# Kernel tuning notes

Hardware: AMD Instinct MI355X
Metric: run time of the kernel (lower is better)

The kernel has to match this reference:

```python
import jax, jax.numpy as jnp
import numpy as np

B, T, WARM, H, FIN, MLPW = 8192, 30, 24, 128, 8, 128
WX = ['clouds','pres','precip','temp','rh','ghi','wind_x','wind_y']
TL = ['hour_sin','hour_cos','year_sin','year_cos','elev_angle','azimuth_sin','azimuth_cos']


def setup_inputs() -> dict:
    key = jax.random.key(0)
    ks = jax.random.split(key, 32)
    d = {}
    for i, n in enumerate(WX + TL):
        d[n] = jax.random.normal(ks[i], (B, T), dtype=jnp.float32)
    d['irradiance_in'] = jax.random.uniform(ks[20], (B, WARM), dtype=jnp.float32)
    s = lambda fan: 1.0 / np.sqrt(fan).astype(np.float32)
    # LSTM params (flax OptimizedLSTMCell math: fused input/hidden kernels, one bias), gate order i,f,g,o
    d['Wi'] = jax.random.normal(ks[21], (FIN, 4 * H), dtype=jnp.float32) * s(FIN)
    d['Wh'] = jax.random.normal(ks[22], (H, 4 * H), dtype=jnp.float32) * s(H)
    d['b'] = jnp.zeros((4 * H,), jnp.float32)
    # output head: MLP(depth=2, width=128) with relu, then Dense(1)
    d['W1'] = jax.random.normal(ks[23], (H, MLPW), dtype=jnp.float32) * s(H)
    d['b1'] = jnp.zeros((MLPW,), jnp.float32)
    d['W2'] = jax.random.normal(ks[24], (MLPW, MLPW), dtype=jnp.float32) * s(MLPW)
    d['b2'] = jnp.zeros((MLPW,), jnp.float32)
    d['Wout'] = jax.random.normal(ks[25], (MLPW, 1), dtype=jnp.float32) * s(MLPW)
    d['bout'] = jnp.zeros((1,), jnp.float32)
    return d


def reference(clouds, pres, precip, temp, rh, ghi, wind_x, wind_y,
              hour_sin, hour_cos, year_sin, year_cos, elev_angle, azimuth_sin, azimuth_cos,
              irradiance_in, Wi, Wh, b, W1, b1, W2, b2, Wout, bout):
    # FLAGS.weather=False path: x is the time/location feature stack [B, T, 7].
    # Weather features are accepted (as in the original dict) but unused.
    x = jnp.stack([hour_sin, hour_cos, year_sin, year_cos, elev_angle, azimuth_sin, azimuth_cos], axis=-1)
    warm_in = jnp.concatenate([x[:, :WARM], irradiance_in[..., None]], axis=-1)  # [B, 24, 8]
    auto_in = x[:, WARM:]                                                        # [B, 6, 7]

    def lstm_step(c, h, inp):
        z = inp @ Wi + h @ Wh + b                    # [B, 4H]
        i, f, g, o = jnp.split(z, 4, axis=-1)
        c2 = jax.nn.sigmoid(f) * c + jax.nn.sigmoid(i) * jnp.tanh(g)
        h2 = jax.nn.sigmoid(o) * jnp.tanh(c2)
        return c2, h2

    def out_mlp(h):
        h = jax.nn.relu(h @ W1 + b1)
        h = jax.nn.relu(h @ W2 + b2)
        return h @ Wout + bout                       # [..., 1]

    c0 = jnp.zeros((x.shape[0], H), x.dtype)
    h0 = jnp.zeros((x.shape[0], H), x.dtype)

    # warmup: teacher-forced LSTM over observed irradiance
    def warm_step(carry, xt):
        c, h = carry
        c, h = lstm_step(c, h, xt)
        return (c, h), h
    (c, h), hs = jax.lax.scan(warm_step, (c0, h0), jnp.swapaxes(warm_in, 0, 1))
    preds_warm = out_mlp(jnp.swapaxes(hs, 0, 1))     # [B, 24, 1]
    last_pred = preds_warm[:, -1]                    # [B, 1]

    def auto_step(carry, xt):
        c, h, p = carry
        c, h = lstm_step(c, h, jnp.concatenate([xt, p], axis=-1))
        p = out_mlp(h)
        return (c, h, p), p
    _, preds_auto = jax.lax.scan(auto_step, (c, h, last_pred), jnp.swapaxes(auto_in, 0, 1))
    preds_auto = jnp.swapaxes(preds_auto, 0, 1)      # [B, 6, 1]

    pred = jnp.concatenate([preds_warm, preds_auto], axis=1)  # [B, 30, 1]
    return jnp.squeeze(pred, axis=2)                 # [B, 30]
```

## Files before the change

### kernel.cpp

```cpp
#include <hip/hip_runtime.h>


#define T_STEPS 30
#define WARM_N  24

typedef _Float16 h8 __attribute__((ext_vector_type(8)));
typedef __attribute__((ext_vector_type(4))) float float4v;

struct FeatPtrs { const float* f[7]; };

#if __has_builtin(__builtin_amdgcn_rcpf)
#define RCP(x) __builtin_amdgcn_rcpf(x)
#else
#define RCP(x) (1.0f/(x))
#endif

__device__ __forceinline__ float sigm(float x){ return RCP(1.0f + __expf(-x)); }
__device__ __forceinline__ float tanh_(float x){ return 1.0f - 2.0f*RCP(1.0f + __expf(2.0f*x)); }

__global__ void pack_weights(const float* __restrict__ Wi, const float* __restrict__ Wh,
                             const float* __restrict__ W1, const float* __restrict__ W2,
                             _Float16* __restrict__ ws)
{
  int idx = blockIdx.x * 256 + threadIdx.x;
  if (idx >= 224 * 512) return;
  int f    = idx >> 9;
  int r    = idx & 511;
  int lane = r >> 3, j = r & 7;
  int kk   = ((lane >> 4) << 3) + j;
  int c16  = lane & 15;
  float v = 0.0f;
  if (f < 160){
    int wt = f / 20, rem = f % 20, g = rem / 5, ks = rem % 5;
    int col = g * 128 + wt * 16 + c16;
    if (ks == 0) v = (kk < 8) ? Wi[kk * 512 + col] : 0.0f;
    else         v = Wh[((ks - 1) * 32 + kk) * 512 + col];
  } else {
    int f2 = f - 160;
    const float* W = (f2 < 32) ? W1 : W2;
    int f3 = f2 & 31;
    int wt = f3 >> 2, ks = f3 & 3;
    v = W[(ks * 32 + kk) * 128 + wt * 16 + c16];
  }
  ws[idx] = (_Float16)v;
}

__device__ __forceinline__ void head_do(int t, int r0, int step,
    const float* o2s, const float* WoutS, float bout0,
    float* __restrict__ out, float* pS)
{
  if (t < 256){
    int r = t >> 3, jj = t & 7;
    const float* orow = &o2s[r * 132 + jj * 16];
    const float* wrow = &WoutS[jj * 16];
    float s = 0.0f;
#pragma unroll
    for (int q = 0; q < 16; ++q) s += orow[q] * wrow[q];
    s += __shfl_down(s, 4, 8);
    s += __shfl_down(s, 2, 8);
    s += __shfl_down(s, 1, 8);
    if (jj == 0){
      float pv = s + bout0;
      out[(r0 + r) * T_STEPS + step] = pv;
      pS[r] = pv;
    }
  }
}

#define MFMA16 __builtin_amdgcn_mfma_f32_16x16x32_f16

__global__ __launch_bounds__(512, 2)
void lstm_mfma(FeatPtrs fp, const float* __restrict__ irr,
               const _Float16* __restrict__ wsb,
               const float* __restrict__ bz, const float* __restrict__ b1,
               const float* __restrict__ b2, const float* __restrict__ Wout,
               const float* __restrict__ bout, float* __restrict__ out)
{
  __shared__ __align__(16) _Float16 xp[2][1280];
  __shared__ __align__(16) _Float16 hp [4 * 1280];
  __shared__ __align__(16) _Float16 o1p[4 * 1280];
  __shared__ __align__(16) float o2s[32 * 132];
  __shared__ float WoutS[128];
  __shared__ float pS[32];

  const int t   = threadIdx.x;
  const int l   = t & 63;
  const int w   = t >> 6;
  const int c16 = l & 15;
  const int kq  = l >> 4;
  const int r0  = blockIdx.x * 32;

  h8 Bz[4][5], B1f[4], B2f[4];
  {
    const h8* f8 = (const h8*)wsb;
#pragma unroll
    for (int g = 0; g < 4; ++g)
#pragma unroll
      for (int ks = 0; ks < 5; ++ks)
        Bz[g][ks] = f8[((w * 4 + g) * 5 + ks) * 64 + l];
#pragma unroll
    for (int ks = 0; ks < 4; ++ks) B1f[ks] = f8[(160 + w * 4 + ks) * 64 + l];
#pragma unroll
    for (int ks = 0; ks < 4; ++ks) B2f[ks] = f8[(192 + w * 4 + ks) * 64 + l];
  }
  float bzv[4], wi7[4];
#pragma unroll
  for (int g = 0; g < 4; ++g){
    bzv[g] = bz[g * 128 + w * 16 + c16];
    wi7[g] = (float)wsb[((w * 4 + g) * 5) * 512 + c16 * 8 + 7];
  }
  const float b1v   = b1[w * 16 + c16];
  const float b2v   = b2[w * 16 + c16];
  const float bout0 = bout[0];
  if (t < 128) WoutS[t] = Wout[t];

  const float* fbase = nullptr;
  const float* ibase = nullptr;
  int xslot = 0;
  if (t < 256){
    int r = t >> 3, j = t & 7;
    if (j < 7) fbase = fp.f[j] + (r0 + r) * T_STEPS;
    else       ibase = irr + (r0 + r) * WARM_N;
    xslot = (r >> 4) * 640 + (r & 15) * 40 + j;
  }

  {
    int* p = (int*)xp;
    for (int i = t; i < 1280; i += 512) p[i] = 0;
    p = (int*)hp;
    for (int i = t; i < 2560; i += 512) p[i] = 0;
  }

  float cst[8];
#pragma unroll
  for (int i = 0; i < 8; ++i) cst[i] = 0.0f;

  const int aoff = c16 * 40 + kq * 8;
  const int wb   = (w >> 1) * 1280 + (w & 1) * 16 + c16;
  __syncthreads();

  if (t < 256){
    float v0 = fbase ? fbase[0] : ibase[0];
    float v1 = fbase ? fbase[1] : ibase[1];
    xp[0][xslot] = (_Float16)v0;
    xp[1][xslot] = (_Float16)v1;
  }
  __syncthreads();

  for (int i = 0; i < 23; ++i){
    float vnext = 0.0f;
    if (t < 256){
      int step = i + 2;
      if (fbase)               vnext = fbase[step];
      else if (step < WARM_N)  vnext = ibase[step];
    }
    float4v acc[4][2];
#pragma unroll
    for (int g = 0; g < 4; ++g)
#pragma unroll
      for (int m = 0; m < 2; ++m)
#pragma unroll
        for (int r = 0; r < 4; ++r) acc[g][m][r] = bzv[g];
    float4v m1[2];
#pragma unroll
    for (int m = 0; m < 2; ++m)
#pragma unroll
      for (int r = 0; r < 4; ++r) m1[m][r] = b1v;
    {
      const _Float16* xb = xp[i & 1];
      h8 a0 = *(const h8*)&xb[aoff];
      h8 a1 = *(const h8*)&xb[640 + aoff];
#pragma unroll
      for (int g = 0; g < 4; ++g){
        acc[g][0] = MFMA16(a0, Bz[g][0], acc[g][0], 0, 0, 0);
        acc[g][1] = MFMA16(a1, Bz[g][0], acc[g][1], 0, 0, 0);
      }
    }
#pragma unroll
    for (int ks = 0; ks < 4; ++ks){
      h8 ah0 = *(const h8*)&hp[ks * 1280 + aoff];
      h8 ah1 = *(const h8*)&hp[ks * 1280 + 640 + aoff];
#pragma unroll
      for (int g = 0; g < 4; ++g){
        acc[g][0] = MFMA16(ah0, Bz[g][1 + ks], acc[g][0], 0, 0, 0);
        acc[g][1] = MFMA16(ah1, Bz[g][1 + ks], acc[g][1], 0, 0, 0);
      }
      if (i >= 1){
        m1[0] = MFMA16(ah0, B1f[ks], m1[0], 0, 0, 0);
        m1[1] = MFMA16(ah1, B1f[ks], m1[1], 0, 0, 0);
      }
    }
    if (i >= 1){
#pragma unroll
      for (int m = 0; m < 2; ++m)
#pragma unroll
        for (int r = 0; r < 4; ++r)
          o1p[wb + m * 640 + (kq * 4 + r) * 40] = (_Float16)fmaxf(m1[m][r], 0.0f);
    }
    if (i >= 2) head_do(t, r0, i - 2, o2s, WoutS, bout0, out, pS);
    __syncthreads();

    if (t < 256) xp[i & 1][xslot] = (_Float16)vnext;
#pragma unroll
    for (int m = 0; m < 2; ++m)
#pragma unroll
      for (int r = 0; r < 4; ++r){
        float zi = acc[0][m][r], zf = acc[1][m][r], zg = acc[2][m][r], zo = acc[3][m][r];
        float c2 = sigm(zf) * cst[m * 4 + r] + sigm(zi) * tanh_(zg);
        cst[m * 4 + r] = c2;
        float h2 = sigm(zo) * tanh_(c2);
        hp[wb + m * 640 + (kq * 4 + r) * 40] = (_Float16)h2;
      }
    if (i >= 1){
      float4v m2[2];
#pragma unroll
      for (int m = 0; m < 2; ++m)
#pragma unroll
        for (int r = 0; r < 4; ++r) m2[m][r] = b2v;
#pragma unroll
      for (int ks = 0; ks < 4; ++ks){
        h8 a0 = *(const h8*)&o1p[ks * 1280 + aoff];
        h8 a1 = *(const h8*)&o1p[ks * 1280 + 640 + aoff];
        m2[0] = MFMA16(a0, B2f[ks], m2[0], 0, 0, 0);
        m2[1] = MFMA16(a1, B2f[ks], m2[1], 0, 0, 0);
      }
#pragma unroll
      for (int m = 0; m < 2; ++m)
#pragma unroll
        for (int r = 0; r < 4; ++r)
          o2s[(m * 16 + kq * 4 + r) * 132 + w * 16 + c16] = fmaxf(m2[m][r], 0.0f);
    }
    __syncthreads();
  }

  head_do(t, r0, 21, o2s, WoutS, bout0, out, pS);
  __syncthreads();

  for (int s = 23; s < T_STEPS; ++s){
    float vnext = 0.0f;
    if (s <= 27 && t < 256 && fbase) vnext = fbase[s + 2];
    float4v acc[4][2];
#pragma unroll
    for (int g = 0; g < 4; ++g)
#pragma unroll
      for (int m = 0; m < 2; ++m)
#pragma unroll
        for (int r = 0; r < 4; ++r) acc[g][m][r] = bzv[g];
    float4v m1[2];
#pragma unroll
    for (int m = 0; m < 2; ++m)
#pragma unroll
      for (int r = 0; r < 4; ++r) m1[m][r] = b1v;
    {
      const _Float16* xb = xp[s & 1];
      h8 a0 = *(const h8*)&xb[aoff];
      h8 a1 = *(const h8*)&xb[640 + aoff];
#pragma unroll
      for (int g = 0; g < 4; ++g){
        acc[g][0] = MFMA16(a0, Bz[g][0], acc[g][0], 0, 0, 0);
        acc[g][1] = MFMA16(a1, Bz[g][0], acc[g][1], 0, 0, 0);
      }
    }
#pragma unroll
    for (int ks = 0; ks < 4; ++ks){
      h8 ah0 = *(const h8*)&hp[ks * 1280 + aoff];
      h8 ah1 = *(const h8*)&hp[ks * 1280 + 640 + aoff];
#pragma unroll
      for (int g = 0; g < 4; ++g){
        acc[g][0] = MFMA16(ah0, Bz[g][1 + ks], acc[g][0], 0, 0, 0);
        acc[g][1] = MFMA16(ah1, Bz[g][1 + ks], acc[g][1], 0, 0, 0);
      }
      m1[0] = MFMA16(ah0, B1f[ks], m1[0], 0, 0, 0);
      m1[1] = MFMA16(ah1, B1f[ks], m1[1], 0, 0, 0);
    }
#pragma unroll
    for (int m = 0; m < 2; ++m)
#pragma unroll
      for (int r = 0; r < 4; ++r)
        o1p[wb + m * 640 + (kq * 4 + r) * 40] = (_Float16)fmaxf(m1[m][r], 0.0f);
    __syncthreads();

    {
      float4v m2[2];
#pragma unroll
      for (int m = 0; m < 2; ++m)
#pragma unroll
        for (int r = 0; r < 4; ++r) m2[m][r] = b2v;
#pragma unroll
      for (int ks = 0; ks < 4; ++ks){
        h8 a0 = *(const h8*)&o1p[ks * 1280 + aoff];
        h8 a1 = *(const h8*)&o1p[ks * 1280 + 640 + aoff];
        m2[0] = MFMA16(a0, B2f[ks], m2[0], 0, 0, 0);
        m2[1] = MFMA16(a1, B2f[ks], m2[1], 0, 0, 0);
      }
#pragma unroll
      for (int m = 0; m < 2; ++m)
#pragma unroll
        for (int r = 0; r < 4; ++r)
          o2s[(m * 16 + kq * 4 + r) * 132 + w * 16 + c16] = fmaxf(m2[m][r], 0.0f);
    }
    __syncthreads();

    head_do(t, r0, s - 1, o2s, WoutS, bout0, out, pS);
    __syncthreads();

    if (s <= 27 && t < 256) xp[s & 1][xslot] = (_Float16)vnext;
    if (s >= 24){
#pragma unroll
      for (int m = 0; m < 2; ++m)
#pragma unroll
        for (int r = 0; r < 4; ++r){
          float pv = pS[m * 16 + kq * 4 + r];
#pragma unroll
          for (int g = 0; g < 4; ++g) acc[g][m][r] += pv * wi7[g];
        }
    }
#pragma unroll
    for (int m = 0; m < 2; ++m)
#pragma unroll
      for (int r = 0; r < 4; ++r){
        float zi = acc[0][m][r], zf = acc[1][m][r], zg = acc[2][m][r], zo = acc[3][m][r];
        float c2 = sigm(zf) * cst[m * 4 + r] + sigm(zi) * tanh_(zg);
        cst[m * 4 + r] = c2;
        float h2 = sigm(zo) * tanh_(c2);
        hp[wb + m * 640 + (kq * 4 + r) * 40] = (_Float16)h2;
      }
    __syncthreads();
  }

  {
    float4v m1[2];
#pragma unroll
    for (int m = 0; m < 2; ++m)
#pragma unroll
      for (int r = 0; r < 4; ++r) m1[m][r] = b1v;
#pragma unroll
    for (int ks = 0; ks < 4; ++ks){
      h8 ah0 = *(const h8*)&hp[ks * 1280 + aoff];
      h8 ah1 = *(const h8*)&hp[ks * 1280 + 640 + aoff];
      m1[0] = MFMA16(ah0, B1f[ks], m1[0], 0, 0, 0);
      m1[1] = MFMA16(ah1, B1f[ks], m1[1], 0, 0, 0);
    }
#pragma unroll
    for (int m = 0; m < 2; ++m)
#pragma unroll
      for (int r = 0; r < 4; ++r)
        o1p[wb + m * 640 + (kq * 4 + r) * 40] = (_Float16)fmaxf(m1[m][r], 0.0f);
    __syncthreads();
    float4v m2[2];
#pragma unroll
    for (int m = 0; m < 2; ++m)
#pragma unroll
      for (int r = 0; r < 4; ++r) m2[m][r] = b2v;
#pragma unroll
    for (int ks = 0; ks < 4; ++ks){
      h8 a0 = *(const h8*)&o1p[ks * 1280 + aoff];
      h8 a1 = *(const h8*)&o1p[ks * 1280 + 640 + aoff];
      m2[0] = MFMA16(a0, B2f[ks], m2[0], 0, 0, 0);
      m2[1] = MFMA16(a1, B2f[ks], m2[1], 0, 0, 0);
    }
#pragma unroll
    for (int m = 0; m < 2; ++m)
#pragma unroll
      for (int r = 0; r < 4; ++r)
        o2s[(m * 16 + kq * 4 + r) * 132 + w * 16 + c16] = fmaxf(m2[m][r], 0.0f);
    __syncthreads();
    head_do(t, r0, 29, o2s, WoutS, bout0, out, pS);
  }
}

extern "C" void kernel_launch(void* const* d_in, const int* in_sizes, int n_in,
                              void* d_out, int out_size, void* d_ws, size_t ws_size,
                              hipStream_t stream)
{
  (void)in_sizes; (void)n_in; (void)out_size; (void)ws_size;
  FeatPtrs fp;
  for (int j = 0; j < 7; ++j) fp.f[j] = (const float*)d_in[8 + j];
  const float* irr  = (const float*)d_in[15];
  const float* Wi   = (const float*)d_in[16];
  const float* Wh   = (const float*)d_in[17];
  const float* bz   = (const float*)d_in[18];
  const float* W1   = (const float*)d_in[19];
  const float* b1   = (const float*)d_in[20];
  const float* W2   = (const float*)d_in[21];
  const float* b2   = (const float*)d_in[22];
  const float* Wout = (const float*)d_in[23];
  const float* bout = (const float*)d_in[24];

  _Float16* ws = (_Float16*)d_ws;
  pack_weights<<<dim3(448), dim3(256), 0, stream>>>(Wi, Wh, W1, W2, ws);
  lstm_mfma<<<dim3(256), dim3(512), 0, stream>>>(
      fp, irr, ws, bz, b1, b2, Wout, bout, (float*)d_out);
}
```

Before: 183.6 us.

## Double-buffer LSTM state and fuse output head into shuffle-reduce atomics

Double-buffers the hidden-state and first-MLP-layer shared buffers and triple-buffers the input tile, so each warmup step needs only one barrier instead of two. The separate head pass that staged the second MLP layer in shared memory and dotted it with Wout is replaced by per-wave multiply with Wout, a cross-lane shuffle reduction and a shared-memory atomicAdd into a per-row accumulator preset to the output bias. The intent is to cut barriers and shared-memory traffic along the serial recurrence. In exchange it adds LDS atomics and more intricate buffer-parity bookkeeping, which risks ordering bugs.

```diff
diff --git a/kernel.cpp b/kernel.cpp
--- a/kernel.cpp
+++ b/kernel.cpp
@@ -45,28 +45,6 @@
   ws[idx] = (_Float16)v;
 }
 
-__device__ __forceinline__ void head_do(int t, int r0, int step,
-    const float* o2s, const float* WoutS, float bout0,
-    float* __restrict__ out, float* pS)
-{
-  if (t < 256){
-    int r = t >> 3, jj = t & 7;
-    const float* orow = &o2s[r * 132 + jj * 16];
-    const float* wrow = &WoutS[jj * 16];
-    float s = 0.0f;
-#pragma unroll
-    for (int q = 0; q < 16; ++q) s += orow[q] * wrow[q];
-    s += __shfl_down(s, 4, 8);
-    s += __shfl_down(s, 2, 8);
-    s += __shfl_down(s, 1, 8);
-    if (jj == 0){
-      float pv = s + bout0;
-      out[(r0 + r) * T_STEPS + step] = pv;
-      pS[r] = pv;
-    }
-  }
-}
-
 #define MFMA16 __builtin_amdgcn_mfma_f32_16x16x32_f16
 
 __global__ __launch_bounds__(512, 2)
@@ -76,12 +54,11 @@
                const float* __restrict__ b2, const float* __restrict__ Wout,
                const float* __restrict__ bout, float* __restrict__ out)
 {
-  __shared__ __align__(16) _Float16 xp[2][1280];
-  __shared__ __align__(16) _Float16 hp [4 * 1280];
-  __shared__ __align__(16) _Float16 o1p[4 * 1280];
-  __shared__ __align__(16) float o2s[32 * 132];
-  __shared__ float WoutS[128];
-  __shared__ float pS[32];
+  __shared__ __align__(16) _Float16 xp[3][1280];
+  __shared__ __align__(16) _Float16 hp[2][5120];
+  __shared__ __align__(16) _Float16 o1p[2][5120];
+  __shared__ float pS[2][32];
+  __shared__ float pSt[32];
 
   const int t   = threadIdx.x;
   const int l   = t & 63;
@@ -112,7 +89,7 @@
   const float b1v   = b1[w * 16 + c16];
   const float b2v   = b2[w * 16 + c16];
   const float bout0 = bout[0];
-  if (t < 128) WoutS[t] = Wout[t];
+  const float woutv = Wout[w * 16 + c16];
 
   const float* fbase = nullptr;
   const float* ibase = nullptr;
@@ -125,10 +102,11 @@
   }
 
   {
-    int* p = (int*)xp;
-    for (int i = t; i < 1280; i += 512) p[i] = 0;
-    p = (int*)hp;
-    for (int i = t; i < 2560; i += 512) p[i] = 0;
+    int* zp = (int*)&xp[0][0];
+    for (int i = t; i < 1920; i += 512) zp[i] = 0;
+    zp = (int*)&hp[0][0];
+    for (int i = t; i < 5120; i += 512) zp[i] = 0;
+    if (t < 64) pS[t >> 5][t & 31] = bout0;
   }
 
   float cst[8];
@@ -141,16 +119,14 @@
 
   if (t < 256){
     float v0 = fbase ? fbase[0] : ibase[0];
-    float v1 = fbase ? fbase[1] : ibase[1];
     xp[0][xslot] = (_Float16)v0;
-    xp[1][xslot] = (_Float16)v1;
   }
   __syncthreads();
 
-  for (int i = 0; i < 23; ++i){
+  for (int i = 0; i < 24; ++i){
     float vnext = 0.0f;
     if (t < 256){
-      int step = i + 2;
+      int step = i + 1;
       if (fbase)               vnext = fbase[step];
       else if (step < WARM_N)  vnext = ibase[step];
     }
@@ -167,7 +143,7 @@
 #pragma unroll
       for (int r = 0; r < 4; ++r) m1[m][r] = b1v;
     {
-      const _Float16* xb = xp[i & 1];
+      const _Float16* xb = xp[i % 3];
       h8 a0 = *(const h8*)&xb[aoff];
       h8 a1 = *(const h8*)&xb[640 + aoff];
 #pragma unroll
@@ -176,69 +152,82 @@
         acc[g][1] = MFMA16(a1, Bz[g][0], acc[g][1], 0, 0, 0);
       }
     }
-#pragma unroll
-    for (int ks = 0; ks < 4; ++ks){
-      h8 ah0 = *(const h8*)&hp[ks * 1280 + aoff];
-      h8 ah1 = *(const h8*)&hp[ks * 1280 + 640 + aoff];
-#pragma unroll
-      for (int g = 0; g < 4; ++g){
-        acc[g][0] = MFMA16(ah0, Bz[g][1 + ks], acc[g][0], 0, 0, 0);
-        acc[g][1] = MFMA16(ah1, Bz[g][1 + ks], acc[g][1], 0, 0, 0);
-      }
-      if (i >= 1){
-        m1[0] = MFMA16(ah0, B1f[ks], m1[0], 0, 0, 0);
-        m1[1] = MFMA16(ah1, B1f[ks], m1[1], 0, 0, 0);
+    {
+      const _Float16* hb = hp[i & 1];
+#pragma unroll
+      for (int ks = 0; ks < 4; ++ks){
+        h8 ah0 = *(const h8*)&hb[ks * 1280 + aoff];
+        h8 ah1 = *(const h8*)&hb[ks * 1280 + 640 + aoff];
+#pragma unroll
+        for (int g = 0; g < 4; ++g){
+          acc[g][0] = MFMA16(ah0, Bz[g][1 + ks], acc[g][0], 0, 0, 0);
+          acc[g][1] = MFMA16(ah1, Bz[g][1 + ks], acc[g][1], 0, 0, 0);
+        }
+        if (i >= 1){
+          m1[0] = MFMA16(ah0, B1f[ks], m1[0], 0, 0, 0);
+          m1[1] = MFMA16(ah1, B1f[ks], m1[1], 0, 0, 0);
+        }
       }
     }
     if (i >= 1){
+      _Float16* o1w = o1p[(i + 1) & 1];
 #pragma unroll
       for (int m = 0; m < 2; ++m)
 #pragma unroll
         for (int r = 0; r < 4; ++r)
-          o1p[wb + m * 640 + (kq * 4 + r) * 40] = (_Float16)fmaxf(m1[m][r], 0.0f);
-    }
-    if (i >= 2) head_do(t, r0, i - 2, o2s, WoutS, bout0, out, pS);
-    __syncthreads();
-
-    if (t < 256) xp[i & 1][xslot] = (_Float16)vnext;
-#pragma unroll
-    for (int m = 0; m < 2; ++m)
-#pragma unroll
-      for (int r = 0; r < 4; ++r){
-        float zi = acc[0][m][r], zf = acc[1][m][r], zg = acc[2][m][r], zo = acc[3][m][r];
-        float c2 = sigm(zf) * cst[m * 4 + r] + sigm(zi) * tanh_(zg);
-        cst[m * 4 + r] = c2;
-        float h2 = sigm(zo) * tanh_(c2);
-        hp[wb + m * 640 + (kq * 4 + r) * 40] = (_Float16)h2;
-      }
-    if (i >= 1){
+          o1w[wb + m * 640 + (kq * 4 + r) * 40] = (_Float16)fmaxf(m1[m][r], 0.0f);
+    }
+    {
+      _Float16* hw = hp[(i + 1) & 1];
+#pragma unroll
+      for (int m = 0; m < 2; ++m)
+#pragma unroll
+        for (int r = 0; r < 4; ++r){
+          float zi = acc[0][m][r], zf = acc[1][m][r], zg = acc[2][m][r], zo = acc[3][m][r];
+          float c2 = sigm(zf) * cst[m * 4 + r] + sigm(zi) * tanh_(zg);
+          cst[m * 4 + r] = c2;
+          float h2 = sigm(zo) * tanh_(c2);
+          hw[wb + m * 640 + (kq * 4 + r) * 40] = (_Float16)h2;
+        }
+    }
+    if (i >= 2){
       float4v m2[2];
 #pragma unroll
       for (int m = 0; m < 2; ++m)
 #pragma unroll
         for (int r = 0; r < 4; ++r) m2[m][r] = b2v;
+      const _Float16* o1r = o1p[i & 1];
 #pragma unroll
       for (int ks = 0; ks < 4; ++ks){
-        h8 a0 = *(const h8*)&o1p[ks * 1280 + aoff];
-        h8 a1 = *(const h8*)&o1p[ks * 1280 + 640 + aoff];
+        h8 a0 = *(const h8*)&o1r[ks * 1280 + aoff];
+        h8 a1 = *(const h8*)&o1r[ks * 1280 + 640 + aoff];
         m2[0] = MFMA16(a0, B2f[ks], m2[0], 0, 0, 0);
         m2[1] = MFMA16(a1, B2f[ks], m2[1], 0, 0, 0);
       }
 #pragma unroll
       for (int m = 0; m < 2; ++m)
 #pragma unroll
-        for (int r = 0; r < 4; ++r)
-          o2s[(m * 16 + kq * 4 + r) * 132 + w * 16 + c16] = fmaxf(m2[m][r], 0.0f);
-    }
-    __syncthreads();
-  }
-
-  head_do(t, r0, 21, o2s, WoutS, bout0, out, pS);
-  __syncthreads();
-
-  for (int s = 23; s < T_STEPS; ++s){
+        for (int r = 0; r < 4; ++r){
+          float v = fmaxf(m2[m][r], 0.0f) * woutv;
+          v += __shfl_xor(v, 1);
+          v += __shfl_xor(v, 2);
+          v += __shfl_xor(v, 4);
+          v += __shfl_xor(v, 8);
+          if (c16 == 0) atomicAdd(&pS[i & 1][m * 16 + kq * 4 + r], v);
+        }
+    }
+    if (i >= 3 && t < 32){
+      float pv = pS[(i + 1) & 1][t];
+      out[(r0 + t) * T_STEPS + (i - 3)] = pv;
+      pS[(i + 1) & 1][t] = bout0;
+    }
+    if (t < 256) xp[(i + 1) % 3][xslot] = (_Float16)vnext;
+    __syncthreads();
+  }
+
+  for (int s = 24; s < T_STEPS; ++s){
     float vnext = 0.0f;
-    if (s <= 27 && t < 256 && fbase) vnext = fbase[s + 2];
+    if (s <= 28 && t < 256 && fbase) vnext = fbase[s + 1];
     float4v acc[4][2];
 #pragma unroll
     for (int g = 0; g < 4; ++g)
@@ -252,7 +241,7 @@
 #pragma unroll
       for (int r = 0; r < 4; ++r) m1[m][r] = b1v;
     {
-      const _Float16* xb = xp[s & 1];
+      const _Float16* xb = xp[s % 3];
       h8 a0 = *(const h8*)&xb[aoff];
       h8 a1 = *(const h8*)&xb[640 + aoff];
 #pragma unroll
@@ -261,111 +250,164 @@
         acc[g][1] = MFMA16(a1, Bz[g][0], acc[g][1], 0, 0, 0);
       }
     }
+    {
+      const _Float16* hb = hp[s & 1];
+#pragma unroll
+      for (int ks = 0; ks < 4; ++ks){
+        h8 ah0 = *(const h8*)&hb[ks * 1280 + aoff];
+        h8 ah1 = *(const h8*)&hb[ks * 1280 + 640 + aoff];
+#pragma unroll
+        for (int g = 0; g < 4; ++g){
+          acc[g][0] = MFMA16(ah0, Bz[g][1 + ks], acc[g][0], 0, 0, 0);
+          acc[g][1] = MFMA16(ah1, Bz[g][1 + ks], acc[g][1], 0, 0, 0);
+        }
+        m1[0] = MFMA16(ah0, B1f[ks], m1[0], 0, 0, 0);
+        m1[1] = MFMA16(ah1, B1f[ks], m1[1], 0, 0, 0);
+      }
+    }
+    {
+      _Float16* o1w = o1p[(s + 1) & 1];
+#pragma unroll
+      for (int m = 0; m < 2; ++m)
+#pragma unroll
+        for (int r = 0; r < 4; ++r)
+          o1w[wb + m * 640 + (kq * 4 + r) * 40] = (_Float16)fmaxf(m1[m][r], 0.0f);
+    }
+    if (s == 24){
+      if (t < 32) out[(r0 + t) * T_STEPS + 21] = pS[1][t];
+      float4v m2[2];
+#pragma unroll
+      for (int m = 0; m < 2; ++m)
+#pragma unroll
+        for (int r = 0; r < 4; ++r) m2[m][r] = b2v;
+      const _Float16* o1r = o1p[0];
+#pragma unroll
+      for (int ks = 0; ks < 4; ++ks){
+        h8 a0 = *(const h8*)&o1r[ks * 1280 + aoff];
+        h8 a1 = *(const h8*)&o1r[ks * 1280 + 640 + aoff];
+        m2[0] = MFMA16(a0, B2f[ks], m2[0], 0, 0, 0);
+        m2[1] = MFMA16(a1, B2f[ks], m2[1], 0, 0, 0);
+      }
+#pragma unroll
+      for (int m = 0; m < 2; ++m)
+#pragma unroll
+        for (int r = 0; r < 4; ++r){
+          float v = fmaxf(m2[m][r], 0.0f) * woutv;
+          v += __shfl_xor(v, 1);
+          v += __shfl_xor(v, 2);
+          v += __shfl_xor(v, 4);
+          v += __shfl_xor(v, 8);
+          if (c16 == 0) atomicAdd(&pS[0][m * 16 + kq * 4 + r], v);
+        }
+    }
+    if (t < 32) pSt[t] = bout0;
+    if (s <= 28 && t < 256) xp[(s + 1) % 3][xslot] = (_Float16)vnext;
+    __syncthreads();
+
+    {
+      float4v m2[2];
+#pragma unroll
+      for (int m = 0; m < 2; ++m)
+#pragma unroll
+        for (int r = 0; r < 4; ++r) m2[m][r] = b2v;
+      const _Float16* o1r = o1p[(s + 1) & 1];
+#pragma unroll
+      for (int ks = 0; ks < 4; ++ks){
+        h8 a0 = *(const h8*)&o1r[ks * 1280 + aoff];
+        h8 a1 = *(const h8*)&o1r[ks * 1280 + 640 + aoff];
+        m2[0] = MFMA16(a0, B2f[ks], m2[0], 0, 0, 0);
+        m2[1] = MFMA16(a1, B2f[ks], m2[1], 0, 0, 0);
+      }
+#pragma unroll
+      for (int m = 0; m < 2; ++m)
+#pragma unroll
+        for (int r = 0; r < 4; ++r){
+          float v = fmaxf(m2[m][r], 0.0f) * woutv;
+          v += __shfl_xor(v, 1);
+          v += __shfl_xor(v, 2);
+          v += __shfl_xor(v, 4);
+          v += __shfl_xor(v, 8);
+          if (c16 == 0) atomicAdd(&pSt[m * 16 + kq * 4 + r], v);
+        }
+    }
+    if (s == 24 && t < 32) out[(r0 + t) * T_STEPS + 22] = pS[0][t];
+    __syncthreads();
+
+#pragma unroll
+    for (int m = 0; m < 2; ++m)
+#pragma unroll
+      for (int r = 0; r < 4; ++r){
+        float pv = pSt[m * 16 + kq * 4 + r];
+#pragma unroll
+        for (int g = 0; g < 4; ++g) acc[g][m][r] += pv * wi7[g];
+      }
+    {
+      _Float16* hw = hp[(s + 1) & 1];
+#pragma unroll
+      for (int m = 0; m < 2; ++m)
+#pragma unroll
+        for (int r = 0; r < 4; ++r){
+          float zi = acc[0][m][r], zf = acc[1][m][r], zg = acc[2][m][r], zo = acc[3][m][r];
+          float c2 = sigm(zf) * cst[m * 4 + r] + sigm(zi) * tanh_(zg);
+          cst[m * 4 + r] = c2;
+          float h2 = sigm(zo) * tanh_(c2);
+          hw[wb + m * 640 + (kq * 4 + r) * 40] = (_Float16)h2;
+        }
+    }
+    if (t < 32) out[(r0 + t) * T_STEPS + (s - 1)] = pSt[t];
+    __syncthreads();
+  }
+
+  {
+    float4v m1[2];
+#pragma unroll
+    for (int m = 0; m < 2; ++m)
+#pragma unroll
+      for (int r = 0; r < 4; ++r) m1[m][r] = b1v;
+    const _Float16* hb = hp[0];
 #pragma unroll
     for (int ks = 0; ks < 4; ++ks){
-      h8 ah0 = *(const h8*)&hp[ks * 1280 + aoff];
-      h8 ah1 = *(const h8*)&hp[ks * 1280 + 640 + aoff];
-#pragma unroll
-      for (int g = 0; g < 4; ++g){
-        acc[g][0] = MFMA16(ah0, Bz[g][1 + ks], acc[g][0], 0, 0, 0);
-        acc[g][1] = MFMA16(ah1, Bz[g][1 + ks], acc[g][1], 0, 0, 0);
-      }
+      h8 ah0 = *(const h8*)&hb[ks * 1280 + aoff];
+      h8 ah1 = *(const h8*)&hb[ks * 1280 + 640 + aoff];
       m1[0] = MFMA16(ah0, B1f[ks], m1[0], 0, 0, 0);
       m1[1] = MFMA16(ah1, B1f[ks], m1[1], 0, 0, 0);
     }
+    _Float16* o1w = o1p[0];
 #pragma unroll
     for (int m = 0; m < 2; ++m)
 #pragma unroll
       for (int r = 0; r < 4; ++r)
-        o1p[wb + m * 640 + (kq * 4 + r) * 40] = (_Float16)fmaxf(m1[m][r], 0.0f);
-    __syncthreads();
-
-    {
-      float4v m2[2];
-#pragma unroll
-      for (int m = 0; m < 2; ++m)
-#pragma unroll
-        for (int r = 0; r < 4; ++r) m2[m][r] = b2v;
-#pragma unroll
-      for (int ks = 0; ks < 4; ++ks){
-        h8 a0 = *(const h8*)&o1p[ks * 1280 + aoff];
-        h8 a1 = *(const h8*)&o1p[ks * 1280 + 640 + aoff];
-        m2[0] = MFMA16(a0, B2f[ks], m2[0], 0, 0, 0);
-        m2[1] = MFMA16(a1, B2f[ks], m2[1], 0, 0, 0);
-      }
-#pragma unroll
-      for (int m = 0; m < 2; ++m)
-#pragma unroll
-        for (int r = 0; r < 4; ++r)
-          o2s[(m * 16 + kq * 4 + r) * 132 + w * 16 + c16] = fmaxf(m2[m][r], 0.0f);
-    }
-    __syncthreads();
-
-    head_do(t, r0, s - 1, o2s, WoutS, bout0, out, pS);
-    __syncthreads();
-
-    if (s <= 27 && t < 256) xp[s & 1][xslot] = (_Float16)vnext;
-    if (s >= 24){
-#pragma unroll
-      for (int m = 0; m < 2; ++m)
-#pragma unroll
-        for (int r = 0; r < 4; ++r){
-          float pv = pS[m * 16 + kq * 4 + r];
-#pragma unroll
-          for (int g = 0; g < 4; ++g) acc[g][m][r] += pv * wi7[g];
-        }
-    }
-#pragma unroll
-    for (int m = 0; m < 2; ++m)
-#pragma unroll
-      for (int r = 0; r < 4; ++r){
-        float zi = acc[0][m][r], zf = acc[1][m][r], zg = acc[2][m][r], zo = acc[3][m][r];
-        float c2 = sigm(zf) * cst[m * 4 + r] + sigm(zi) * tanh_(zg);
-        cst[m * 4 + r] = c2;
-        float h2 = sigm(zo) * tanh_(c2);
-        hp[wb + m * 640 + (kq * 4 + r) * 40] = (_Float16)h2;
-      }
-    __syncthreads();
-  }
-
-  {
-    float4v m1[2];
-#pragma unroll
-    for (int m = 0; m < 2; ++m)
-#pragma unroll
-      for (int r = 0; r < 4; ++r) m1[m][r] = b1v;
+        o1w[wb + m * 640 + (kq * 4 + r) * 40] = (_Float16)fmaxf(m1[m][r], 0.0f);
+    if (t < 32) pSt[t] = bout0;
+    __syncthreads();
+
+    float4v m2[2];
+#pragma unroll
+    for (int m = 0; m < 2; ++m)
+#pragma unroll
+      for (int r = 0; r < 4; ++r) m2[m][r] = b2v;
+    const _Float16* o1r = o1p[0];
 #pragma unroll
     for (int ks = 0; ks < 4; ++ks){
-      h8 ah0 = *(const h8*)&hp[ks * 1280 + aoff];
-      h8 ah1 = *(const h8*)&hp[ks * 1280 + 640 + aoff];
-      m1[0] = MFMA16(ah0, B1f[ks], m1[0], 0, 0, 0);
-      m1[1] = MFMA16(ah1, B1f[ks], m1[1], 0, 0, 0);
-    }
-#pragma unroll
-    for (int m = 0; m < 2; ++m)
-#pragma unroll
-      for (int r = 0; r < 4; ++r)
-        o1p[wb + m * 640 + (kq * 4 + r) * 40] = (_Float16)fmaxf(m1[m][r], 0.0f);
-    __syncthreads();
-    float4v m2[2];
-#pragma unroll
-    for (int m = 0; m < 2; ++m)
-#pragma unroll
-      for (int r = 0; r < 4; ++r) m2[m][r] = b2v;
-#pragma unroll
-    for (int ks = 0; ks < 4; ++ks){
-      h8 a0 = *(const h8*)&o1p[ks * 1280 + aoff];
-      h8 a1 = *(const h8*)&o1p[ks * 1280 + 640 + aoff];
+      h8 a0 = *(const h8*)&o1r[ks * 1280 + aoff];
+      h8 a1 = *(const h8*)&o1r[ks * 1280 + 640 + aoff];
       m2[0] = MFMA16(a0, B2f[ks], m2[0], 0, 0, 0);
       m2[1] = MFMA16(a1, B2f[ks], m2[1], 0, 0, 0);
     }
 #pragma unroll
     for (int m = 0; m < 2; ++m)
 #pragma unroll
-      for (int r = 0; r < 4; ++r)
-        o2s[(m * 16 + kq * 4 + r) * 132 + w * 16 + c16] = fmaxf(m2[m][r], 0.0f);
-    __syncthreads();
-    head_do(t, r0, 29, o2s, WoutS, bout0, out, pS);
+      for (int r = 0; r < 4; ++r){
+        float v = fmaxf(m2[m][r], 0.0f) * woutv;
+        v += __shfl_xor(v, 1);
+        v += __shfl_xor(v, 2);
+        v += __shfl_xor(v, 4);
+        v += __shfl_xor(v, 8);
+        if (c16 == 0) atomicAdd(&pSt[m * 16 + kq * 4 + r], v);
+      }
+    __syncthreads();
+
+    if (t < 32) out[(r0 + t) * T_STEPS + 29] = pSt[t];
   }
 }
 
```

After: 213.1 us. +16.1%, slower.

## Software-pipeline warmup LSTM across two row halves to overlap MFMA and gates

Applied to the files above, without the earlier changes.

Splits the 32-row block into two 16-row halves and staggers them in the warmup loop. While one half runs its gate and hidden MFMAs, the other half does its sigmoid/tanh gate math, second MLP layer and output head, with one barrier per half-step. This is meant to hide the transcendental and LDS latency behind matrix work within a wave, and to cut per-step serialization. The cost is more barriers per timestep (two half-steps instead of two full phases), more complex prologue and epilogue code, and possible extra register pressure from two accumulator sets.

```diff
diff --git a/kernel.cpp b/kernel.cpp
--- a/kernel.cpp
+++ b/kernel.cpp
@@ -45,29 +45,67 @@
   ws[idx] = (_Float16)v;
 }
 
-__device__ __forceinline__ void head_do(int t, int r0, int step,
-    const float* o2s, const float* WoutS, float bout0,
-    float* __restrict__ out, float* pS)
-{
-  if (t < 256){
-    int r = t >> 3, jj = t & 7;
-    const float* orow = &o2s[r * 132 + jj * 16];
-    const float* wrow = &WoutS[jj * 16];
-    float s = 0.0f;
-#pragma unroll
-    for (int q = 0; q < 16; ++q) s += orow[q] * wrow[q];
-    s += __shfl_down(s, 4, 8);
-    s += __shfl_down(s, 2, 8);
-    s += __shfl_down(s, 1, 8);
-    if (jj == 0){
-      float pv = s + bout0;
-      out[(r0 + r) * T_STEPS + step] = pv;
-      pS[r] = pv;
-    }
-  }
-}
-
 #define MFMA16 __builtin_amdgcn_mfma_f32_16x16x32_f16
+
+#define INIT_ACC(ACC) \
+  _Pragma("unroll") for (int g_ = 0; g_ < 4; ++g_) \
+    _Pragma("unroll") for (int r_ = 0; r_ < 4; ++r_) ACC[g_][r_] = bzv[g_];
+
+#define INIT4(V, B) \
+  _Pragma("unroll") for (int r_ = 0; r_ < 4; ++r_) V[r_] = (B);
+
+#define ZA(ACC, M1V, XBUF, HOFF, DO1) \
+  { h8 ax_ = *(const h8*)&xp[XBUF][(HOFF) + aoff]; \
+    _Pragma("unroll") for (int g_ = 0; g_ < 4; ++g_) \
+      ACC[g_] = MFMA16(ax_, Bz[g_][0], ACC[g_], 0, 0, 0); } \
+  _Pragma("unroll") for (int ks_ = 0; ks_ < 4; ++ks_){ \
+    h8 ah_ = *(const h8*)&hp[ks_ * 1280 + (HOFF) + aoff]; \
+    _Pragma("unroll") for (int g_ = 0; g_ < 4; ++g_) \
+      ACC[g_] = MFMA16(ah_, Bz[g_][1 + ks_], ACC[g_], 0, 0, 0); \
+    if (DO1) M1V = MFMA16(ah_, B1f[ks_], M1V, 0, 0, 0); }
+
+#define WRITE_O1(M1V, HOFF) \
+  _Pragma("unroll") for (int r_ = 0; r_ < 4; ++r_) \
+    o1p[wb + (HOFF) + (kq * 4 + r_) * 40] = (_Float16)fmaxf(M1V[r_], 0.0f);
+
+#define GATES(ACC, CB, HOFF) \
+  _Pragma("unroll") for (int r_ = 0; r_ < 4; ++r_){ \
+    float zi_ = ACC[0][r_], zf_ = ACC[1][r_], zg_ = ACC[2][r_], zo_ = ACC[3][r_]; \
+    float c2_ = sigm(zf_) * cst[(CB) + r_] + sigm(zi_) * tanh_(zg_); \
+    cst[(CB) + r_] = c2_; \
+    float h2_ = sigm(zo_) * tanh_(c2_); \
+    hp[wb + (HOFF) + (kq * 4 + r_) * 40] = (_Float16)h2_; }
+
+#define DO_MLP2(HOFF, ROWB) \
+  { float4v m2_; INIT4(m2_, b2v) \
+    _Pragma("unroll") for (int ks_ = 0; ks_ < 4; ++ks_){ \
+      h8 a_ = *(const h8*)&o1p[ks_ * 1280 + (HOFF) + aoff]; \
+      m2_ = MFMA16(a_, B2f[ks_], m2_, 0, 0, 0); } \
+    _Pragma("unroll") for (int r_ = 0; r_ < 4; ++r_) \
+      o2s[((ROWB) + kq * 4 + r_) * 132 + w * 16 + c16] = fmaxf(m2_[r_], 0.0f); }
+
+#define HEAD_HALF(TLO, RB, STEP) \
+  if (t >= (TLO) && t < (TLO) + 128){ \
+    int r_ = (RB) + ((t - (TLO)) >> 3), jj_ = t & 7; \
+    const float* orow_ = &o2s[r_ * 132 + jj_ * 16]; \
+    const float* wrow_ = &WoutS[jj_ * 16]; \
+    float s_ = 0.0f; \
+    _Pragma("unroll") for (int q_ = 0; q_ < 16; ++q_) s_ += orow_[q_] * wrow_[q_]; \
+    s_ += __shfl_down(s_, 4, 8); s_ += __shfl_down(s_, 2, 8); s_ += __shfl_down(s_, 1, 8); \
+    if (jj_ == 0){ float pv_ = s_ + bout0; \
+      out[(r0 + r_) * T_STEPS + (STEP)] = pv_; pS[r_] = pv_; } }
+
+#define STAGE_WARM(STEP, BUF) \
+  if (t < 256){ \
+    float v_ = 0.0f; \
+    if (fbase) v_ = fbase[STEP]; \
+    else if ((STEP) < WARM_N) v_ = ibase[STEP]; \
+    xp[BUF][xslot] = (_Float16)v_; }
+
+#define STAGE_TAIL(STEP, BUF) \
+  if (t < 256){ \
+    float v_ = fbase ? fbase[STEP] : 0.0f; \
+    xp[BUF][xslot] = (_Float16)v_; }
 
 __global__ __launch_bounds__(512, 2)
 void lstm_mfma(FeatPtrs fp, const float* __restrict__ irr,
@@ -125,10 +163,10 @@
   }
 
   {
-    int* p = (int*)xp;
-    for (int i = t; i < 1280; i += 512) p[i] = 0;
-    p = (int*)hp;
-    for (int i = t; i < 2560; i += 512) p[i] = 0;
+    int* zp = (int*)&xp[0][0];
+    for (int i = t; i < 1280; i += 512) zp[i] = 0;
+    zp = (int*)hp;
+    for (int i = t; i < 2560; i += 512) zp[i] = 0;
   }
 
   float cst[8];
@@ -141,19 +179,70 @@
 
   if (t < 256){
     float v0 = fbase ? fbase[0] : ibase[0];
-    float v1 = fbase ? fbase[1] : ibase[1];
     xp[0][xslot] = (_Float16)v0;
-    xp[1][xslot] = (_Float16)v1;
-  }
-  __syncthreads();
-
-  for (int i = 0; i < 23; ++i){
-    float vnext = 0.0f;
-    if (t < 256){
-      int step = i + 2;
-      if (fbase)               vnext = fbase[step];
-      else if (step < WARM_N)  vnext = ibase[step];
-    }
+  }
+  __syncthreads();
+
+  float4v acc0[4], acc1[4];
+  float4v m1a, m1b;
+
+  STAGE_WARM(1, 1)
+  INIT_ACC(acc0)
+  ZA(acc0, m1a, 0, 0, 0)
+  __syncthreads();
+
+  INIT_ACC(acc1)
+  ZA(acc1, m1b, 0, 640, 0)
+  GATES(acc0, 0, 0)
+  __syncthreads();
+
+  STAGE_WARM(2, 0)
+  INIT_ACC(acc0)
+  INIT4(m1a, b1v)
+  ZA(acc0, m1a, 1, 0, 1)
+  WRITE_O1(m1a, 0)
+  GATES(acc1, 4, 640)
+  __syncthreads();
+
+  INIT_ACC(acc1)
+  INIT4(m1b, b1v)
+  ZA(acc1, m1b, 1, 640, 1)
+  WRITE_O1(m1b, 640)
+  GATES(acc0, 0, 0)
+  DO_MLP2(0, 0)
+  __syncthreads();
+
+  for (int i = 2; i < 24; ++i){
+    const int xbi = i & 1, xbo = (i + 1) & 1;
+    STAGE_WARM(i + 1, xbo)
+    INIT_ACC(acc0)
+    INIT4(m1a, b1v)
+    ZA(acc0, m1a, xbi, 0, 1)
+    WRITE_O1(m1a, 0)
+    GATES(acc1, 4, 640)
+    DO_MLP2(640, 16)
+    HEAD_HALF(0, 0, i - 2)
+    __syncthreads();
+
+    INIT_ACC(acc1)
+    INIT4(m1b, b1v)
+    ZA(acc1, m1b, xbi, 640, 1)
+    WRITE_O1(m1b, 640)
+    GATES(acc0, 0, 0)
+    DO_MLP2(0, 0)
+    HEAD_HALF(128, 16, i - 2)
+    __syncthreads();
+  }
+
+  GATES(acc1, 4, 640)
+  DO_MLP2(640, 16)
+  HEAD_HALF(0, 0, 22)
+  __syncthreads();
+  HEAD_HALF(128, 16, 22)
+  __syncthreads();
+
+  for (int s = 24; s < T_STEPS; ++s){
+    if (s <= 28){ STAGE_TAIL(s + 1, (s + 1) & 1) }
     float4v acc[4][2];
 #pragma unroll
     for (int g = 0; g < 4; ++g)
@@ -167,7 +256,7 @@
 #pragma unroll
       for (int r = 0; r < 4; ++r) m1[m][r] = b1v;
     {
-      const _Float16* xb = xp[i & 1];
+      const _Float16* xb = xp[s & 1];
       h8 a0 = *(const h8*)&xb[aoff];
       h8 a1 = *(const h8*)&xb[640 + aoff];
 #pragma unroll
@@ -185,22 +274,32 @@
         acc[g][0] = MFMA16(ah0, Bz[g][1 + ks], acc[g][0], 0, 0, 0);
         acc[g][1] = MFMA16(ah1, Bz[g][1 + ks], acc[g][1], 0, 0, 0);
       }
-      if (i >= 1){
-        m1[0] = MFMA16(ah0, B1f[ks], m1[0], 0, 0, 0);
-        m1[1] = MFMA16(ah1, B1f[ks], m1[1], 0, 0, 0);
+      m1[0] = MFMA16(ah0, B1f[ks], m1[0], 0, 0, 0);
+      m1[1] = MFMA16(ah1, B1f[ks], m1[1], 0, 0, 0);
+    }
+#pragma unroll
+    for (int m = 0; m < 2; ++m)
+#pragma unroll
+      for (int r = 0; r < 4; ++r)
+        o1p[wb + m * 640 + (kq * 4 + r) * 40] = (_Float16)fmaxf(m1[m][r], 0.0f);
+    __syncthreads();
+
+    DO_MLP2(0, 0)
+    DO_MLP2(640, 16)
+    __syncthreads();
+
+    HEAD_HALF(0, 0, s - 1)
+    HEAD_HALF(128, 16, s - 1)
+    __syncthreads();
+
+#pragma unroll
+    for (int m = 0; m < 2; ++m)
+#pragma unroll
+      for (int r = 0; r < 4; ++r){
+        float pv = pS[m * 16 + kq * 4 + r];
+#pragma unroll
+        for (int g = 0; g < 4; ++g) acc[g][m][r] += pv * wi7[g];
       }
-    }
-    if (i >= 1){
-#pragma unroll
-      for (int m = 0; m < 2; ++m)
-#pragma unroll
-        for (int r = 0; r < 4; ++r)
-          o1p[wb + m * 640 + (kq * 4 + r) * 40] = (_Float16)fmaxf(m1[m][r], 0.0f);
-    }
-    if (i >= 2) head_do(t, r0, i - 2, o2s, WoutS, bout0, out, pS);
-    __syncthreads();
-
-    if (t < 256) xp[i & 1][xslot] = (_Float16)vnext;
 #pragma unroll
     for (int m = 0; m < 2; ++m)
 #pragma unroll
@@ -211,120 +310,6 @@
         float h2 = sigm(zo) * tanh_(c2);
         hp[wb + m * 640 + (kq * 4 + r) * 40] = (_Float16)h2;
       }
-    if (i >= 1){
-      float4v m2[2];
-#pragma unroll
-      for (int m = 0; m < 2; ++m)
-#pragma unroll
-        for (int r = 0; r < 4; ++r) m2[m][r] = b2v;
-#pragma unroll
-      for (int ks = 0; ks < 4; ++ks){
-        h8 a0 = *(const h8*)&o1p[ks * 1280 + aoff];
-        h8 a1 = *(const h8*)&o1p[ks * 1280 + 640 + aoff];
-        m2[0] = MFMA16(a0, B2f[ks], m2[0], 0, 0, 0);
-        m2[1] = MFMA16(a1, B2f[ks], m2[1], 0, 0, 0);
-      }
-#pragma unroll
-      for (int m = 0; m < 2; ++m)
-#pragma unroll
-        for (int r = 0; r < 4; ++r)
-          o2s[(m * 16 + kq * 4 + r) * 132 + w * 16 + c16] = fmaxf(m2[m][r], 0.0f);
-    }
-    __syncthreads();
-  }
-
-  head_do(t, r0, 21, o2s, WoutS, bout0, out, pS);
-  __syncthreads();
-
-  for (int s = 23; s < T_STEPS; ++s){
-    float vnext = 0.0f;
-    if (s <= 27 && t < 256 && fbase) vnext = fbase[s + 2];
-    float4v acc[4][2];
-#pragma unroll
-    for (int g = 0; g < 4; ++g)
-#pragma unroll
-      for (int m = 0; m < 2; ++m)
-#pragma unroll
-        for (int r = 0; r < 4; ++r) acc[g][m][r] = bzv[g];
-    float4v m1[2];
-#pragma unroll
-    for (int m = 0; m < 2; ++m)
-#pragma unroll
-      for (int r = 0; r < 4; ++r) m1[m][r] = b1v;
-    {
-      const _Float16* xb = xp[s & 1];
-      h8 a0 = *(const h8*)&xb[aoff];
-      h8 a1 = *(const h8*)&xb[640 + aoff];
-#pragma unroll
-      for (int g = 0; g < 4; ++g){
-        acc[g][0] = MFMA16(a0, Bz[g][0], acc[g][0], 0, 0, 0);
-        acc[g][1] = MFMA16(a1, Bz[g][0], acc[g][1], 0, 0, 0);
-      }
-    }
-#pragma unroll
-    for (int ks = 0; ks < 4; ++ks){
-      h8 ah0 = *(const h8*)&hp[ks * 1280 + aoff];
-      h8 ah1 = *(const h8*)&hp[ks * 1280 + 640 + aoff];
-#pragma unroll
-      for (int g = 0; g < 4; ++g){
-        acc[g][0] = MFMA16(ah0, Bz[g][1 + ks], acc[g][0], 0, 0, 0);
-        acc[g][1] = MFMA16(ah1, Bz[g][1 + ks], acc[g][1], 0, 0, 0);
-      }
-      m1[0] = MFMA16(ah0, B1f[ks], m1[0], 0, 0, 0);
-      m1[1] = MFMA16(ah1, B1f[ks], m1[1], 0, 0, 0);
-    }
-#pragma unroll
-    for (int m = 0; m < 2; ++m)
-#pragma unroll
-      for (int r = 0; r < 4; ++r)
-        o1p[wb + m * 640 + (kq * 4 + r) * 40] = (_Float16)fmaxf(m1[m][r], 0.0f);
-    __syncthreads();
-
-    {
-      float4v m2[2];
-#pragma unroll
-      for (int m = 0; m < 2; ++m)
-#pragma unroll
-        for (int r = 0; r < 4; ++r) m2[m][r] = b2v;
-#pragma unroll
-      for (int ks = 0; ks < 4; ++ks){
-        h8 a0 = *(const h8*)&o1p[ks * 1280 + aoff];
-        h8 a1 = *(const h8*)&o1p[ks * 1280 + 640 + aoff];
-        m2[0] = MFMA16(a0, B2f[ks], m2[0], 0, 0, 0);
-        m2[1] = MFMA16(a1, B2f[ks], m2[1], 0, 0, 0);
-      }
-#pragma unroll
-      for (int m = 0; m < 2; ++m)
-#pragma unroll
-        for (int r = 0; r < 4; ++r)
-          o2s[(m * 16 + kq * 4 + r) * 132 + w * 16 + c16] = fmaxf(m2[m][r], 0.0f);
-    }
-    __syncthreads();
-
-    head_do(t, r0, s - 1, o2s, WoutS, bout0, out, pS);
-    __syncthreads();
-
-    if (s <= 27 && t < 256) xp[s & 1][xslot] = (_Float16)vnext;
-    if (s >= 24){
-#pragma unroll
-      for (int m = 0; m < 2; ++m)
-#pragma unroll
-        for (int r = 0; r < 4; ++r){
-          float pv = pS[m * 16 + kq * 4 + r];
-#pragma unroll
-          for (int g = 0; g < 4; ++g) acc[g][m][r] += pv * wi7[g];
-        }
-    }
-#pragma unroll
-    for (int m = 0; m < 2; ++m)
-#pragma unroll
-      for (int r = 0; r < 4; ++r){
-        float zi = acc[0][m][r], zf = acc[1][m][r], zg = acc[2][m][r], zo = acc[3][m][r];
-        float c2 = sigm(zf) * cst[m * 4 + r] + sigm(zi) * tanh_(zg);
-        cst[m * 4 + r] = c2;
-        float h2 = sigm(zo) * tanh_(c2);
-        hp[wb + m * 640 + (kq * 4 + r) * 40] = (_Float16)h2;
-      }
     __syncthreads();
   }
 
@@ -347,25 +332,11 @@
       for (int r = 0; r < 4; ++r)
         o1p[wb + m * 640 + (kq * 4 + r) * 40] = (_Float16)fmaxf(m1[m][r], 0.0f);
     __syncthreads();
-    float4v m2[2];
-#pragma unroll
-    for (int m = 0; m < 2; ++m)
-#pragma unroll
-      for (int r = 0; r < 4; ++r) m2[m][r] = b2v;
-#pragma unroll
-    for (int ks = 0; ks < 4; ++ks){
-      h8 a0 = *(const h8*)&o1p[ks * 1280 + aoff];
-      h8 a1 = *(const h8*)&o1p[ks * 1280 + 640 + aoff];
-      m2[0] = MFMA16(a0, B2f[ks], m2[0], 0, 0, 0);
-      m2[1] = MFMA16(a1, B2f[ks], m2[1], 0, 0, 0);
-    }
-#pragma unroll
-    for (int m = 0; m < 2; ++m)
-#pragma unroll
-      for (int r = 0; r < 4; ++r)
-        o2s[(m * 16 + kq * 4 + r) * 132 + w * 16 + c16] = fmaxf(m2[m][r], 0.0f);
-    __syncthreads();
-    head_do(t, r0, 29, o2s, WoutS, bout0, out, pS);
+    DO_MLP2(0, 0)
+    DO_MLP2(640, 16)
+    __syncthreads();
+    HEAD_HALF(0, 0, 29)
+    HEAD_HALF(128, 16, 29)
   }
 }
 
```

Measured after the change: 178.1 us (median of 2 runs). -3.0%, faster.
